# Kernel tuning notes

Measured on AMD Instinct MI355X. Metric: run time of the kernel, lower is better.

## Reference

```python
import jax, jax.numpy as jnp
import numpy as np

B, N_, K_, Q_, H = 32, 20, 10, 2048, 1024
EPS = 1e-5  # torch LayerNorm default


def setup_inputs() -> dict:
    key = jax.random.key(0)
    k1, k2 = jax.random.split(key)
    return {
        "support": jax.random.normal(k1, (B * N_ * K_, H), dtype=jnp.float32),
        "query": jax.random.normal(k2, (B * Q_, H), dtype=jnp.float32),
        "gamma": jnp.ones((H,), dtype=jnp.float32),
        "beta": jnp.zeros((H,), dtype=jnp.float32),
        "N": N_,
        "K": K_,
        "Q_total": Q_,
    }


def _layernorm(x, gamma, beta):
    m = jnp.mean(x, axis=-1, keepdims=True)
    v = jnp.mean(jnp.square(x - m), axis=-1, keepdims=True)  # biased variance
    return (x - m) * jax.lax.rsqrt(v + EPS) * gamma + beta


def reference(support, query, gamma, beta, N, K, Q_total):
    H_ = gamma.shape[0]
    s = _layernorm(support, gamma, beta).reshape(-1, N * K, H_)   # (B, NK, H)
    q = _layernorm(query, gamma, beta).reshape(-1, Q_total, H_)   # (B, Q, H)
    # broadcast dot-product similarity, fused as a batched matmul
    z = jnp.einsum("bqh,bkh->bqk", q, s)                          # (B, Q, NK)
    z = z.reshape(-1, Q_total, N, K)
    logits = jnp.max(z, axis=-1)                                  # max over K -> (B, Q, N)
    minn = jnp.min(logits, axis=-1)                               # min over N -> (B, Q)
    logits = jnp.concatenate([logits, minn[:, :, None] - 1.0], axis=2)  # (B, Q, N+1)
    pred = jnp.argmax(logits.reshape(-1, N + 1), axis=1)
    return logits, pred
```

## Files before the change

### kernel.cpp

```cpp
#include <hip/hip_runtime.h>
#include <hip/hip_bf16.h>

#define Hd   1024
#define Bd   32
#define Nd   20
#define Kd   10
#define NKd  200
#define NKP  208
#define Qd   2048
#define BM   128
#define ZR   64
#define ZLD  209
#define EPSf 1e-5f
#define TAU  0.02f
#define MAXF 2048
#define TCH  (832 * 8)
#define PLB  (TCH * 2)
#define BUFB (2 * PLB)

typedef __attribute__((ext_vector_type(8))) short bf16x8;
typedef __attribute__((ext_vector_type(4))) float f32x4;
typedef __attribute__((ext_vector_type(4))) unsigned int u32x4;

#define SWS(r) (((r) ^ ((r) >> 2)) & 3)

static __device__ __forceinline__ unsigned short f2bf(float f) {
  union { float f; unsigned u; } c; c.f = f;
  unsigned r = c.u + 0x7FFFu + ((c.u >> 16) & 1u);
  return (unsigned short)(r >> 16);
}
static __device__ __forceinline__ float bf2f(unsigned short h) {
  union { unsigned u; float f; } c; c.u = ((unsigned)h) << 16;
  return c.f;
}
static __device__ __forceinline__ float ubitf(unsigned u) {
  union { unsigned u; float f; } c; c.u = u; return c.f;
}
static __device__ __forceinline__ unsigned cvtpk_bf16(float a, float b) {
  unsigned r;
  asm("v_cvt_pk_bf16_f32 %0, %1, %2" : "=v"(r) : "v"(a), "v"(b));
  return r;
}
static __device__ __forceinline__ void gload_lds16(const void* g, void* l) {
  __builtin_amdgcn_global_load_lds(
      (const __attribute__((address_space(1))) unsigned int*)g,
      (__attribute__((address_space(3))) unsigned int*)l, 16, 0, 0);
}

__global__ __launch_bounds__(256) void ln_support(const float* __restrict__ x,
                                                  const float* __restrict__ gamma,
                                                  const float* __restrict__ beta,
                                                  unsigned short* __restrict__ y_hi,
                                                  unsigned short* __restrict__ y_lo,
                                                  float* __restrict__ Gv,
                                                  float* __restrict__ Bv) {
  int wave = threadIdx.x >> 6, lane = threadIdx.x & 63;
  int p = blockIdx.x * 4 + wave;
  int b = p / NKP, rr = p - b * NKP;
  int T0 = lane >> 1;
  int k8base = (lane & 1) * 2;
  int sw = SWS(rr);
  size_t chunkbase = (size_t)b * 32 * TCH + (size_t)T0 * TCH + (size_t)rr * 32;

  if (rr >= NKd) {
    bf16x8 z8 = {0, 0, 0, 0, 0, 0, 0, 0};
#pragma unroll
    for (int pr = 0; pr < 2; ++pr) {
      size_t off = chunkbase + (size_t)(((k8base + pr) ^ sw) * 8);
      *(bf16x8*)(y_hi + off) = z8;
      *(bf16x8*)(y_lo + off) = z8;
    }
    if (lane == 0) { Gv[p] = 0.f; Bv[p] = 0.f; }
    return;
  }
  const float4* xr = (const float4*)(x + ((size_t)b * NKd + rr) * Hd);
  const float4* gr = (const float4*)gamma;
  const float4* br = (const float4*)beta;
  float4 v[4];
  float s = 0.f, ss = 0.f;
#pragma unroll
  for (int j = 0; j < 4; ++j) {
    v[j] = xr[lane * 4 + j];
    s  += v[j].x + v[j].y + v[j].z + v[j].w;
    ss += v[j].x * v[j].x + v[j].y * v[j].y + v[j].z * v[j].z + v[j].w * v[j].w;
  }
#pragma unroll
  for (int o = 32; o; o >>= 1) { s += __shfl_xor(s, o, 64); ss += __shfl_xor(ss, o, 64); }
  float mean = s * (1.0f / Hd);
  float rstd = rsqrtf(ss * (1.0f / Hd) - mean * mean + EPSf);

  float nx[16];
  float sg = 0.f, sb = 0.f;
#pragma unroll
  for (int j = 0; j < 4; ++j) {
    float4 g = gr[lane * 4 + j], bb = br[lane * 4 + j];
    float xv[4] = {v[j].x, v[j].y, v[j].z, v[j].w};
    float gv4[4] = {g.x, g.y, g.z, g.w};
    float bv4[4] = {bb.x, bb.y, bb.z, bb.w};
#pragma unroll
    for (int e = 0; e < 4; ++e) {
      float n = (xv[e] - mean) * rstd * gv4[e] + bv4[e];
      nx[j * 4 + e] = n;
      sg += n * gv4[e];
      sb += n * bv4[e];
    }
  }
#pragma unroll
  for (int pr = 0; pr < 2; ++pr) {
    bf16x8 ph, pl;
#pragma unroll
    for (int e = 0; e < 8; ++e) {
      float n = nx[pr * 8 + e];
      unsigned short h = f2bf(n);
      ph[e] = (short)h;
      pl[e] = (short)f2bf(n - bf2f(h));
    }
    size_t off = chunkbase + (size_t)(((k8base + pr) ^ sw) * 8);
    *(bf16x8*)(y_hi + off) = ph;
    *(bf16x8*)(y_lo + off) = pl;
  }
#pragma unroll
  for (int o = 32; o; o >>= 1) { sg += __shfl_xor(sg, o, 64); sb += __shfl_xor(sb, o, 64); }
  if (lane == 0) { Gv[p] = sg; Bv[p] = sb; }
}

static __device__ __forceinline__ void split8(float4 xa, float4 xb, float4 ga, float4 gb,
                                              float& sx, float& sxx,
                                              bf16x8& AH, bf16x8& AL) {
  float x[8] = {xa.x, xa.y, xa.z, xa.w, xb.x, xb.y, xb.z, xb.w};
  float g[8] = {ga.x, ga.y, ga.z, ga.w, gb.x, gb.y, gb.z, gb.w};
  float u[8];
#pragma unroll
  for (int e = 0; e < 8; ++e) {
    sx += x[e];
    sxx = fmaf(x[e], x[e], sxx);
    u[e] = x[e] * g[e];
  }
  unsigned h[4], l[4];
#pragma unroll
  for (int p = 0; p < 4; ++p) {
    h[p] = cvtpk_bf16(u[2 * p], u[2 * p + 1]);
    float r0 = ubitf(h[p] << 16);
    float r1 = ubitf(h[p] & 0xFFFF0000u);
    l[p] = cvtpk_bf16(u[2 * p] - r0, u[2 * p + 1] - r1);
  }
  AH = __builtin_bit_cast(bf16x8, (u32x4){h[0], h[1], h[2], h[3]});
  AL = __builtin_bit_cast(bf16x8, (u32x4){l[0], l[1], l[2], l[3]});
}

__global__ __launch_bounds__(256, 2) void gemm_reduce(
    const float* __restrict__ query,
    const unsigned short* __restrict__ s_hi, const unsigned short* __restrict__ s_lo,
    const float* __restrict__ gamma,
    const float* __restrict__ Gv, const float* __restrict__ Bv,
    float* __restrict__ out_logits, float* __restrict__ out_pred,
    int* __restrict__ flag_cnt, int* __restrict__ flag_list) {
  __shared__ __align__(16) union {
    unsigned short B[2][2][TCH];
    float z[ZR][ZLD];
  } sm;

  int lin = blockIdx.x;
  int xcd = lin & 7, sl = lin >> 3;
  int b = xcd + 8 * (sl >> 4);
  int m0 = (sl & 15) * BM;
  int t = threadIdx.x;
  int wave = t >> 6, lane = t & 63;
  int m = lane & 15, quad = lane >> 4;

  const size_t qrow0 = (size_t)b * Qd + m0;
  const float* qf0 = query + (qrow0 + wave * 32 + m) * Hd;
  const float* qf1 = qf0 + 16 * Hd;
  const unsigned short* hb = s_hi + (size_t)b * 32 * TCH;
  const unsigned short* lb = s_lo + (size_t)b * 32 * TCH;

  char* ldsB = (char*)&sm.B[0][0][0];
  const char* rdB = ldsB + m * 64 + ((quad ^ SWS(m)) * 16);

  auto issue_dma = [&](int Tn, int bufsel) {
    size_t toff = (size_t)Tn * TCH;
    char* dstb = ldsB + bufsel * BUFB;
#pragma unroll
    for (int i = 0; i < 7; ++i) {
      int j = wave + i * 4;
      if (j < 26) {
        int pl = j >= 13 ? 1 : 0, jj = j - pl * 13;
        const unsigned short* src = (pl ? lb : hb) + toff + (size_t)jj * 512 + lane * 8;
        gload_lds16(src, dstb + pl * PLB + jj * 1024);
      }
    }
  };

  float4 xq00, xq01, xq10, xq11, gq0, gq1;
  auto loadA = [&](int T) {
    int ko = T * 32 + quad * 8;
    const float4* g4 = (const float4*)(gamma + ko);
    gq0 = g4[0]; gq1 = g4[1];
    const float4* q0 = (const float4*)(qf0 + ko);
    xq00 = q0[0]; xq01 = q0[1];
    const float4* q1 = (const float4*)(qf1 + ko);
    xq10 = q1[0]; xq11 = q1[1];
  };

  f32x4 acc0[13], acc1[13];
#pragma unroll
  for (int i = 0; i < 13; ++i) {
    acc0[i] = (f32x4){0.f, 0.f, 0.f, 0.f};
    acc1[i] = (f32x4){0.f, 0.f, 0.f, 0.f};
  }
  float sx0 = 0.f, sxx0 = 0.f, sx1 = 0.f, sxx1 = 0.f;

  issue_dma(0, 0);
  loadA(0);

  for (int T = 0; T < 32; ++T) {
    int u = T & 1;
    __syncthreads();

    if (T + 1 < 32) issue_dma(T + 1, 1 - u);

    bf16x8 ah0, al0, ah1, al1;
    split8(xq00, xq01, gq0, gq1, sx0, sxx0, ah0, al0);
    split8(xq10, xq11, gq0, gq1, sx1, sxx1, ah1, al1);
    if (T + 1 < 32) loadA(T + 1);

    const char* Bu = rdB + (u ? BUFB : 0);
#pragma unroll
    for (int nt = 0; nt < 13; ++nt) {
      bf16x8 bh = *(const bf16x8*)(Bu + nt * 1024);
      bf16x8 bl = *(const bf16x8*)(Bu + PLB + nt * 1024);
      acc0[nt] = __builtin_amdgcn_mfma_f32_16x16x32_bf16(ah0, bh, acc0[nt], 0, 0, 0);
      acc1[nt] = __builtin_amdgcn_mfma_f32_16x16x32_bf16(ah1, bh, acc1[nt], 0, 0, 0);
      acc0[nt] = __builtin_amdgcn_mfma_f32_16x16x32_bf16(al0, bh, acc0[nt], 0, 0, 0);
      acc1[nt] = __builtin_amdgcn_mfma_f32_16x16x32_bf16(al1, bh, acc1[nt], 0, 0, 0);
      acc0[nt] = __builtin_amdgcn_mfma_f32_16x16x32_bf16(ah0, bl, acc0[nt], 0, 0, 0);
      acc1[nt] = __builtin_amdgcn_mfma_f32_16x16x32_bf16(ah1, bl, acc1[nt], 0, 0, 0);
    }
  }

  sx0 += __shfl_xor(sx0, 16, 64);  sxx0 += __shfl_xor(sxx0, 16, 64);
  sx0 += __shfl_xor(sx0, 32, 64);  sxx0 += __shfl_xor(sxx0, 32, 64);
  sx1 += __shfl_xor(sx1, 16, 64);  sxx1 += __shfl_xor(sxx1, 16, 64);
  sx1 += __shfl_xor(sx1, 32, 64);  sxx1 += __shfl_xor(sxx1, 32, 64);
  float mean0 = sx0 * (1.0f / Hd);
  float rstd0 = rsqrtf(sxx0 * (1.0f / Hd) - mean0 * mean0 + EPSf);
  float mean1 = sx1 * (1.0f / Hd);
  float rstd1 = rsqrtf(sxx1 * (1.0f / Hd) - mean1 * mean1 + EPSf);

  float Gc[13], Bc[13];
#pragma unroll
  for (int nt = 0; nt < 13; ++nt) {
    int col = b * NKP + nt * 16 + m;
    Gc[nt] = Gv[col];
    Bc[nt] = Bv[col];
  }

#pragma unroll
  for (int pass = 0; pass < 2; ++pass) {
    __syncthreads();
    if ((wave >> 1) == pass) {
      int zb = (wave & 1) * 32;
#pragma unroll
      for (int r = 0; r < 4; ++r) {
        int lr = quad * 4 + r;
        {
          float mn = __shfl(mean0, lr, 16), rs = __shfl(rstd0, lr, 16);
          float mrs = mn * rs;
#pragma unroll
          for (int nt = 0; nt < 13; ++nt)
            sm.z[zb + lr][nt * 16 + m] = rs * acc0[nt][r] - mrs * Gc[nt] + Bc[nt];
        }
        {
          float mn = __shfl(mean1, lr, 16), rs = __shfl(rstd1, lr, 16);
          float mrs = mn * rs;
#pragma unroll
          for (int nt = 0; nt < 13; ++nt)
            sm.z[zb + 16 + lr][nt * 16 + m] = rs * acc1[nt][r] - mrs * Gc[nt] + Bc[nt];
        }
      }
    }
    __syncthreads();

    for (int i = t; i < ZR * Nd; i += 256) {
      int row = i / Nd, g = i - row * Nd;
      float* zp = &sm.z[row][g * Kd];
      float mx = zp[0];
#pragma unroll
      for (int j = 1; j < Kd; ++j) mx = fmaxf(mx, zp[j]);
      zp[0] = mx;
    }
    __syncthreads();

    if (t < ZR) {
      int row = t;
      float mn = 3.4e38f, v1 = -3.4e38f, v2 = -3.4e38f;
      int best = 0;
      size_t orow = qrow0 + pass * ZR + row;
      float* lp = out_logits + orow * (Nd + 1);
#pragma unroll
      for (int n = 0; n < Nd; ++n) {
        float v = sm.z[row][n * Kd];
        lp[n] = v;
        mn = fminf(mn, v);
        if (v > v1) { v2 = v1; v1 = v; best = n; }
        else v2 = fmaxf(v2, v);
      }
      lp[Nd] = mn - 1.0f;
      out_pred[orow] = (float)best;
      if (v1 - v2 < TAU) {
        int idx = atomicAdd(flag_cnt, 1);
        if (idx < MAXF) flag_list[idx] = (int)orow;
      }
    }
  }
}

__global__ __launch_bounds__(256) void refine_pred(
    const float* __restrict__ query, const float* __restrict__ support,
    const float* __restrict__ gamma, const float* __restrict__ beta,
    const int* __restrict__ flag_cnt, const int* __restrict__ flag_list,
    float* __restrict__ out_pred) {
  __shared__ double A[Hd];
  __shared__ double red[16];
  __shared__ double zbuf[NKd];
  __shared__ double gmax[Nd];
  int cnt = *flag_cnt; if (cnt > MAXF) cnt = MAXF;
  if ((int)blockIdx.x >= cnt) return;
  int qrow = flag_list[blockIdx.x];
  int b = qrow / Qd;
  int t = threadIdx.x, lane = t & 63, w = t >> 6;
  const float* qx = query + (size_t)qrow * Hd;
  float xv[4];
  double sx = 0.0, sxx = 0.0;
#pragma unroll
  for (int i = 0; i < 4; ++i) {
    xv[i] = qx[t * 4 + i];
    sx += (double)xv[i]; sxx += (double)xv[i] * (double)xv[i];
  }
#pragma unroll
  for (int o = 32; o; o >>= 1) { sx += __shfl_xor(sx, o, 64); sxx += __shfl_xor(sxx, o, 64); }
  if (lane == 0) { red[w] = sx; red[8 + w] = sxx; }
  __syncthreads();
  double m = (red[0] + red[1] + red[2] + red[3]) * (1.0 / Hd);
  double var = (red[8] + red[9] + red[10] + red[11]) * (1.0 / Hd) - m * m;
  double r = 1.0 / sqrt(var + 1e-5);
  double s1 = 0.0, s2 = 0.0;
#pragma unroll
  for (int i = 0; i < 4; ++i) {
    int j = t * 4 + i;
    double g = (double)gamma[j], be = (double)beta[j];
    double qn = ((double)xv[i] - m) * r * g + be;
    double a = qn * g;
    A[j] = a; s1 += a; s2 += qn * be;
  }
#pragma unroll
  for (int o = 32; o; o >>= 1) { s1 += __shfl_xor(s1, o, 64); s2 += __shfl_xor(s2, o, 64); }
  __syncthreads();
  if (lane == 0) { red[w] = s1; red[8 + w] = s2; }
  __syncthreads();
  double S1 = red[0] + red[1] + red[2] + red[3];
  double S2 = red[8] + red[9] + red[10] + red[11];
  const float* sbase = support + (size_t)b * NKd * Hd;
  for (int row = w; row < NKd; row += 4) {
    const float* xr = sbase + (size_t)row * Hd;
    double tx = 0.0, txx = 0.0, tax = 0.0;
#pragma unroll
    for (int i = 0; i < 16; ++i) {
      int j = lane + i * 64;
      double x = (double)xr[j];
      tx += x; txx += x * x; tax += A[j] * x;
    }
#pragma unroll
    for (int o = 32; o; o >>= 1) {
      tx += __shfl_xor(tx, o, 64); txx += __shfl_xor(txx, o, 64); tax += __shfl_xor(tax, o, 64);
    }
    if (lane == 0) {
      double mm = tx * (1.0 / Hd);
      double vv = txx * (1.0 / Hd) - mm * mm;
      double rr = 1.0 / sqrt(vv + 1e-5);
      zbuf[row] = rr * (tax - mm * S1) + S2;
    }
  }
  __syncthreads();
  if (t < Nd) {
    double mx = zbuf[t * Kd];
#pragma unroll
    for (int j = 1; j < Kd; ++j) mx = fmax(mx, zbuf[t * Kd + j]);
    gmax[t] = mx;
  }
  __syncthreads();
  if (t == 0) {
    double bv = gmax[0]; int best = 0;
#pragma unroll
    for (int n = 1; n < Nd; ++n) if (gmax[n] > bv) { bv = gmax[n]; best = n; }
    out_pred[qrow] = (float)best;
  }
}

extern "C" void kernel_launch(void* const* d_in, const int* in_sizes, int n_in,
                              void* d_out, int out_size, void* d_ws, size_t ws_size,
                              hipStream_t stream) {
  const float* support = (const float*)d_in[0];
  const float* query   = (const float*)d_in[1];
  const float* gamma   = (const float*)d_in[2];
  const float* beta    = (const float*)d_in[3];

  float* out = (float*)d_out;
  float* out_logits = out;
  float* out_pred   = out + (size_t)Bd * Qd * (Nd + 1);

  const size_t plane = (size_t)Bd * 32 * TCH;
  unsigned short* s_hi = (unsigned short*)d_ws;
  unsigned short* s_lo = s_hi + plane;
  char* p = (char*)(s_lo + plane);
  float* Gv = (float*)p;            p += (size_t)Bd * NKP * sizeof(float);
  float* Bv = (float*)p;            p += (size_t)Bd * NKP * sizeof(float);
  int* flag_cnt = (int*)p;
  int* flag_list = (int*)(p + 256);

  hipMemsetAsync(flag_cnt, 0, sizeof(int), stream);
  ln_support<<<(Bd * NKP) / 4, 256, 0, stream>>>(support, gamma, beta, s_hi, s_lo, Gv, Bv);
  gemm_reduce<<<Qd / BM * Bd, 256, 0, stream>>>(query, s_hi, s_lo, gamma, Gv, Bv,
                                                out_logits, out_pred, flag_cnt, flag_list);
  refine_pred<<<MAXF, 256, 0, stream>>>(query, support, gamma, beta, flag_cnt, flag_list, out_pred);
}
```

Baseline: 488.3 us.

## Triple-buffer support tiles with explicit vmcnt waits and prefetch distance two

```diff
diff --git a/kernel.cpp b/kernel.cpp
--- a/kernel.cpp
+++ b/kernel.cpp
@@ -156,9 +156,10 @@
     float* __restrict__ out_logits, float* __restrict__ out_pred,
     int* __restrict__ flag_cnt, int* __restrict__ flag_list) {
   __shared__ __align__(16) union {
-    unsigned short B[2][2][TCH];
+    unsigned short B[3][2][TCH];
     float z[ZR][ZLD];
   } sm;
+  __shared__ __align__(16) char dma_pad[1024];
 
   int lin = blockIdx.x;
   int xcd = lin & 7, sl = lin >> 3;
@@ -183,11 +184,12 @@
 #pragma unroll
     for (int i = 0; i < 7; ++i) {
       int j = wave + i * 4;
-      if (j < 26) {
-        int pl = j >= 13 ? 1 : 0, jj = j - pl * 13;
-        const unsigned short* src = (pl ? lb : hb) + toff + (size_t)jj * 512 + lane * 8;
-        gload_lds16(src, dstb + pl * PLB + jj * 1024);
-      }
+      bool real = (j < 26);
+      int pl = (real && j >= 13) ? 1 : 0;
+      int jj = real ? (j - pl * 13) : 0;
+      const unsigned short* src = (pl ? lb : hb) + toff + (size_t)jj * 512 + lane * 8;
+      void* dst = real ? (void*)(dstb + pl * PLB + jj * 1024) : (void*)dma_pad;
+      gload_lds16(src, dst);
     }
   };
 
@@ -211,20 +213,33 @@
   float sx0 = 0.f, sxx0 = 0.f, sx1 = 0.f, sxx1 = 0.f;
 
   issue_dma(0, 0);
+  __builtin_amdgcn_sched_barrier(0);
+  asm volatile("" ::: "memory");
   loadA(0);
-
+  __builtin_amdgcn_sched_barrier(0);
+  asm volatile("" ::: "memory");
+  issue_dma(1, 1);
+
+  int bu = 0;
   for (int T = 0; T < 32; ++T) {
-    int u = T & 1;
-    __syncthreads();
-
-    if (T + 1 < 32) issue_dma(T + 1, 1 - u);
+    if (T < 31) asm volatile("s_waitcnt vmcnt(13)" ::: "memory");
+    else        asm volatile("s_waitcnt vmcnt(6)" ::: "memory");
+    __builtin_amdgcn_s_barrier();
+    __builtin_amdgcn_sched_barrier(0);
 
     bf16x8 ah0, al0, ah1, al1;
     split8(xq00, xq01, gq0, gq1, sx0, sxx0, ah0, al0);
     split8(xq10, xq11, gq0, gq1, sx1, sxx1, ah1, al1);
     if (T + 1 < 32) loadA(T + 1);
-
-    const char* Bu = rdB + (u ? BUFB : 0);
+    __builtin_amdgcn_sched_barrier(0);
+    asm volatile("" ::: "memory");
+    if (T + 2 < 32) {
+      int bd = bu + 2; if (bd >= 3) bd -= 3;
+      issue_dma(T + 2, bd);
+    }
+
+    const char* Bu = rdB + bu * BUFB;
+    __builtin_amdgcn_s_setprio(1);
 #pragma unroll
     for (int nt = 0; nt < 13; ++nt) {
       bf16x8 bh = *(const bf16x8*)(Bu + nt * 1024);
@@ -236,6 +251,8 @@
       acc0[nt] = __builtin_amdgcn_mfma_f32_16x16x32_bf16(ah0, bl, acc0[nt], 0, 0, 0);
       acc1[nt] = __builtin_amdgcn_mfma_f32_16x16x32_bf16(ah1, bl, acc1[nt], 0, 0, 0);
     }
+    __builtin_amdgcn_s_setprio(0);
+    if (++bu == 3) bu = 0;
   }
 
   sx0 += __shfl_xor(sx0, 16, 64);  sxx0 += __shfl_xor(sxx0, 16, 64);
```

Result: slower. 499.8 us (+2.4%).

## Halve query tile per block, single-buffer LDS, raise occupancy to four blocks

Applied to the files above, without the earlier changes.

```diff
diff --git a/kernel.cpp b/kernel.cpp
--- a/kernel.cpp
+++ b/kernel.cpp
@@ -8,15 +8,14 @@
 #define NKd  200
 #define NKP  208
 #define Qd   2048
-#define BM   128
-#define ZR   64
+#define BM   64
+#define ZR   32
 #define ZLD  209
 #define EPSf 1e-5f
 #define TAU  0.02f
 #define MAXF 2048
 #define TCH  (832 * 8)
 #define PLB  (TCH * 2)
-#define BUFB (2 * PLB)
 
 typedef __attribute__((ext_vector_type(8))) short bf16x8;
 typedef __attribute__((ext_vector_type(4))) float f32x4;
@@ -148,7 +147,7 @@
   AL = __builtin_bit_cast(bf16x8, (u32x4){l[0], l[1], l[2], l[3]});
 }
 
-__global__ __launch_bounds__(256, 2) void gemm_reduce(
+__global__ __launch_bounds__(256, 4) void gemm_reduce(
     const float* __restrict__ query,
     const unsigned short* __restrict__ s_hi, const unsigned short* __restrict__ s_lo,
     const float* __restrict__ gamma,
@@ -156,96 +155,78 @@
     float* __restrict__ out_logits, float* __restrict__ out_pred,
     int* __restrict__ flag_cnt, int* __restrict__ flag_list) {
   __shared__ __align__(16) union {
-    unsigned short B[2][2][TCH];
+    unsigned short Bb[2][TCH];
     float z[ZR][ZLD];
   } sm;
 
   int lin = blockIdx.x;
   int xcd = lin & 7, sl = lin >> 3;
-  int b = xcd + 8 * (sl >> 4);
-  int m0 = (sl & 15) * BM;
+  int b = xcd + 8 * (sl >> 5);
+  int m0 = (sl & 31) * BM;
   int t = threadIdx.x;
   int wave = t >> 6, lane = t & 63;
   int m = lane & 15, quad = lane >> 4;
 
   const size_t qrow0 = (size_t)b * Qd + m0;
-  const float* qf0 = query + (qrow0 + wave * 32 + m) * Hd;
-  const float* qf1 = qf0 + 16 * Hd;
+  const float* qf0 = query + (qrow0 + wave * 16 + m) * Hd;
   const unsigned short* hb = s_hi + (size_t)b * 32 * TCH;
   const unsigned short* lb = s_lo + (size_t)b * 32 * TCH;
 
-  char* ldsB = (char*)&sm.B[0][0][0];
+  char* ldsB = (char*)&sm.Bb[0][0];
   const char* rdB = ldsB + m * 64 + ((quad ^ SWS(m)) * 16);
 
-  auto issue_dma = [&](int Tn, int bufsel) {
+  auto issue_dma = [&](int Tn) {
     size_t toff = (size_t)Tn * TCH;
-    char* dstb = ldsB + bufsel * BUFB;
-#pragma unroll
-    for (int i = 0; i < 7; ++i) {
-      int j = wave + i * 4;
-      if (j < 26) {
-        int pl = j >= 13 ? 1 : 0, jj = j - pl * 13;
-        const unsigned short* src = (pl ? lb : hb) + toff + (size_t)jj * 512 + lane * 8;
-        gload_lds16(src, dstb + pl * PLB + jj * 1024);
-      }
+    for (int j = wave; j < 26; j += 4) {
+      int pl = j >= 13 ? 1 : 0, jj = j - pl * 13;
+      const unsigned short* src = (pl ? lb : hb) + toff + (size_t)jj * 512 + lane * 8;
+      gload_lds16(src, ldsB + pl * PLB + jj * 1024);
     }
   };
 
-  float4 xq00, xq01, xq10, xq11, gq0, gq1;
+  float4 xq0, xq1, gq0, gq1;
   auto loadA = [&](int T) {
     int ko = T * 32 + quad * 8;
     const float4* g4 = (const float4*)(gamma + ko);
     gq0 = g4[0]; gq1 = g4[1];
     const float4* q0 = (const float4*)(qf0 + ko);
-    xq00 = q0[0]; xq01 = q0[1];
-    const float4* q1 = (const float4*)(qf1 + ko);
-    xq10 = q1[0]; xq11 = q1[1];
+    xq0 = q0[0]; xq1 = q0[1];
   };
 
-  f32x4 acc0[13], acc1[13];
-#pragma unroll
-  for (int i = 0; i < 13; ++i) {
-    acc0[i] = (f32x4){0.f, 0.f, 0.f, 0.f};
-    acc1[i] = (f32x4){0.f, 0.f, 0.f, 0.f};
-  }
-  float sx0 = 0.f, sxx0 = 0.f, sx1 = 0.f, sxx1 = 0.f;
-
-  issue_dma(0, 0);
+  f32x4 acc[13];
+#pragma unroll
+  for (int i = 0; i < 13; ++i) acc[i] = (f32x4){0.f, 0.f, 0.f, 0.f};
+  float sx = 0.f, sxx = 0.f;
+
+  issue_dma(0);
   loadA(0);
 
   for (int T = 0; T < 32; ++T) {
-    int u = T & 1;
-    __syncthreads();
-
-    if (T + 1 < 32) issue_dma(T + 1, 1 - u);
-
-    bf16x8 ah0, al0, ah1, al1;
-    split8(xq00, xq01, gq0, gq1, sx0, sxx0, ah0, al0);
-    split8(xq10, xq11, gq0, gq1, sx1, sxx1, ah1, al1);
+    __syncthreads();
+
+    bf16x8 ah, al;
+    split8(xq0, xq1, gq0, gq1, sx, sxx, ah, al);
     if (T + 1 < 32) loadA(T + 1);
 
-    const char* Bu = rdB + (u ? BUFB : 0);
+    __builtin_amdgcn_s_setprio(1);
 #pragma unroll
     for (int nt = 0; nt < 13; ++nt) {
-      bf16x8 bh = *(const bf16x8*)(Bu + nt * 1024);
-      bf16x8 bl = *(const bf16x8*)(Bu + PLB + nt * 1024);
-      acc0[nt] = __builtin_amdgcn_mfma_f32_16x16x32_bf16(ah0, bh, acc0[nt], 0, 0, 0);
-      acc1[nt] = __builtin_amdgcn_mfma_f32_16x16x32_bf16(ah1, bh, acc1[nt], 0, 0, 0);
-      acc0[nt] = __builtin_amdgcn_mfma_f32_16x16x32_bf16(al0, bh, acc0[nt], 0, 0, 0);
-      acc1[nt] = __builtin_amdgcn_mfma_f32_16x16x32_bf16(al1, bh, acc1[nt], 0, 0, 0);
-      acc0[nt] = __builtin_amdgcn_mfma_f32_16x16x32_bf16(ah0, bl, acc0[nt], 0, 0, 0);
-      acc1[nt] = __builtin_amdgcn_mfma_f32_16x16x32_bf16(ah1, bl, acc1[nt], 0, 0, 0);
-    }
-  }
-
-  sx0 += __shfl_xor(sx0, 16, 64);  sxx0 += __shfl_xor(sxx0, 16, 64);
-  sx0 += __shfl_xor(sx0, 32, 64);  sxx0 += __shfl_xor(sxx0, 32, 64);
-  sx1 += __shfl_xor(sx1, 16, 64);  sxx1 += __shfl_xor(sxx1, 16, 64);
-  sx1 += __shfl_xor(sx1, 32, 64);  sxx1 += __shfl_xor(sxx1, 32, 64);
-  float mean0 = sx0 * (1.0f / Hd);
-  float rstd0 = rsqrtf(sxx0 * (1.0f / Hd) - mean0 * mean0 + EPSf);
-  float mean1 = sx1 * (1.0f / Hd);
-  float rstd1 = rsqrtf(sxx1 * (1.0f / Hd) - mean1 * mean1 + EPSf);
+      bf16x8 bh = *(const bf16x8*)(rdB + nt * 1024);
+      bf16x8 bl = *(const bf16x8*)(rdB + PLB + nt * 1024);
+      acc[nt] = __builtin_amdgcn_mfma_f32_16x16x32_bf16(ah, bh, acc[nt], 0, 0, 0);
+      acc[nt] = __builtin_amdgcn_mfma_f32_16x16x32_bf16(al, bh, acc[nt], 0, 0, 0);
+      acc[nt] = __builtin_amdgcn_mfma_f32_16x16x32_bf16(ah, bl, acc[nt], 0, 0, 0);
+    }
+    __builtin_amdgcn_s_setprio(0);
+
+    __syncthreads();
+    if (T + 1 < 32) issue_dma(T + 1);
+  }
+
+  sx += __shfl_xor(sx, 16, 64);  sxx += __shfl_xor(sxx, 16, 64);
+  sx += __shfl_xor(sx, 32, 64);  sxx += __shfl_xor(sxx, 32, 64);
+  float mean = sx * (1.0f / Hd);
+  float rstd = rsqrtf(sxx * (1.0f / Hd) - mean * mean + EPSf);
 
   float Gc[13], Bc[13];
 #pragma unroll
@@ -259,24 +240,15 @@
   for (int pass = 0; pass < 2; ++pass) {
     __syncthreads();
     if ((wave >> 1) == pass) {
-      int zb = (wave & 1) * 32;
+      int zb = (wave & 1) * 16;
 #pragma unroll
       for (int r = 0; r < 4; ++r) {
         int lr = quad * 4 + r;
-        {
-          float mn = __shfl(mean0, lr, 16), rs = __shfl(rstd0, lr, 16);
-          float mrs = mn * rs;
-#pragma unroll
-          for (int nt = 0; nt < 13; ++nt)
-            sm.z[zb + lr][nt * 16 + m] = rs * acc0[nt][r] - mrs * Gc[nt] + Bc[nt];
-        }
-        {
-          float mn = __shfl(mean1, lr, 16), rs = __shfl(rstd1, lr, 16);
-          float mrs = mn * rs;
-#pragma unroll
-          for (int nt = 0; nt < 13; ++nt)
-            sm.z[zb + 16 + lr][nt * 16 + m] = rs * acc1[nt][r] - mrs * Gc[nt] + Bc[nt];
-        }
+        float mn = __shfl(mean, lr, 16), rs = __shfl(rstd, lr, 16);
+        float mrs = mn * rs;
+#pragma unroll
+        for (int nt = 0; nt < 13; ++nt)
+          sm.z[zb + lr][nt * 16 + m] = rs * acc[nt][r] - mrs * Gc[nt] + Bc[nt];
       }
     }
     __syncthreads();
```

Measured after the change: 490.8 us. About the same (+0.5%).

## Interleave DMA issue and MFMA phases with barriers and priority hints

Applied to the files above, without the earlier changes.

```diff
diff --git a/kernel.cpp b/kernel.cpp
--- a/kernel.cpp
+++ b/kernel.cpp
@@ -148,6 +148,8 @@
   AL = __builtin_bit_cast(bf16x8, (u32x4){l[0], l[1], l[2], l[3]});
 }
 
+#define MFMA_BF16 __builtin_amdgcn_mfma_f32_16x16x32_bf16
+
 __global__ __launch_bounds__(256, 2) void gemm_reduce(
     const float* __restrict__ query,
     const unsigned short* __restrict__ s_hi, const unsigned short* __restrict__ s_lo,
@@ -177,11 +179,11 @@
   char* ldsB = (char*)&sm.B[0][0][0];
   const char* rdB = ldsB + m * 64 + ((quad ^ SWS(m)) * 16);
 
-  auto issue_dma = [&](int Tn, int bufsel) {
+  auto issue_dma_phase = [&](int Tn, int bufsel, int p) {
     size_t toff = (size_t)Tn * TCH;
     char* dstb = ldsB + bufsel * BUFB;
 #pragma unroll
-    for (int i = 0; i < 7; ++i) {
+    for (int i = p; i < 7; i += 4) {
       int j = wave + i * 4;
       if (j < 26) {
         int pl = j >= 13 ? 1 : 0, jj = j - pl * 13;
@@ -210,31 +212,66 @@
   }
   float sx0 = 0.f, sxx0 = 0.f, sx1 = 0.f, sxx1 = 0.f;
 
-  issue_dma(0, 0);
+#pragma unroll
+  for (int p = 0; p < 4; ++p) issue_dma_phase(0, 0, p);
   loadA(0);
 
   for (int T = 0; T < 32; ++T) {
     int u = T & 1;
     __syncthreads();
 
-    if (T + 1 < 32) issue_dma(T + 1, 1 - u);
-
     bf16x8 ah0, al0, ah1, al1;
     split8(xq00, xq01, gq0, gq1, sx0, sxx0, ah0, al0);
     split8(xq10, xq11, gq0, gq1, sx1, sxx1, ah1, al1);
-    if (T + 1 < 32) loadA(T + 1);
 
     const char* Bu = rdB + (u ? BUFB : 0);
-#pragma unroll
-    for (int nt = 0; nt < 13; ++nt) {
-      bf16x8 bh = *(const bf16x8*)(Bu + nt * 1024);
-      bf16x8 bl = *(const bf16x8*)(Bu + PLB + nt * 1024);
-      acc0[nt] = __builtin_amdgcn_mfma_f32_16x16x32_bf16(ah0, bh, acc0[nt], 0, 0, 0);
-      acc1[nt] = __builtin_amdgcn_mfma_f32_16x16x32_bf16(ah1, bh, acc1[nt], 0, 0, 0);
-      acc0[nt] = __builtin_amdgcn_mfma_f32_16x16x32_bf16(al0, bh, acc0[nt], 0, 0, 0);
-      acc1[nt] = __builtin_amdgcn_mfma_f32_16x16x32_bf16(al1, bh, acc1[nt], 0, 0, 0);
-      acc0[nt] = __builtin_amdgcn_mfma_f32_16x16x32_bf16(ah0, bl, acc0[nt], 0, 0, 0);
-      acc1[nt] = __builtin_amdgcn_mfma_f32_16x16x32_bf16(ah1, bl, acc1[nt], 0, 0, 0);
+
+    {
+      bf16x8 bh[4], bl[4];
+#pragma unroll
+      for (int i = 0; i < 4; ++i) {
+        bh[i] = *(const bf16x8*)(Bu + i * 1024);
+        bl[i] = *(const bf16x8*)(Bu + PLB + i * 1024);
+      }
+      if (T + 1 < 32) { issue_dma_phase(T + 1, 1 - u, 0); loadA(T + 1); }
+      __builtin_amdgcn_s_barrier();
+      __builtin_amdgcn_sched_barrier(0);
+      __builtin_amdgcn_s_setprio(1);
+#pragma unroll
+      for (int i = 0; i < 4; ++i) {
+        acc0[i] = MFMA_BF16(ah0, bh[i], acc0[i], 0, 0, 0);
+        acc1[i] = MFMA_BF16(ah1, bh[i], acc1[i], 0, 0, 0);
+        acc0[i] = MFMA_BF16(al0, bh[i], acc0[i], 0, 0, 0);
+        acc1[i] = MFMA_BF16(al1, bh[i], acc1[i], 0, 0, 0);
+        acc0[i] = MFMA_BF16(ah0, bl[i], acc0[i], 0, 0, 0);
+        acc1[i] = MFMA_BF16(ah1, bl[i], acc1[i], 0, 0, 0);
+      }
+      __builtin_amdgcn_s_setprio(0);
+    }
+#pragma unroll
+    for (int p = 1; p < 4; ++p) {
+      int base = 1 + p * 3;
+      bf16x8 bh[3], bl[3];
+#pragma unroll
+      for (int i = 0; i < 3; ++i) {
+        bh[i] = *(const bf16x8*)(Bu + (base + i) * 1024);
+        bl[i] = *(const bf16x8*)(Bu + PLB + (base + i) * 1024);
+      }
+      if (T + 1 < 32) issue_dma_phase(T + 1, 1 - u, p);
+      __builtin_amdgcn_s_barrier();
+      __builtin_amdgcn_sched_barrier(0);
+      __builtin_amdgcn_s_setprio(1);
+#pragma unroll
+      for (int i = 0; i < 3; ++i) {
+        int nt = base + i;
+        acc0[nt] = MFMA_BF16(ah0, bh[i], acc0[nt], 0, 0, 0);
+        acc1[nt] = MFMA_BF16(ah1, bh[i], acc1[nt], 0, 0, 0);
+        acc0[nt] = MFMA_BF16(al0, bh[i], acc0[nt], 0, 0, 0);
+        acc1[nt] = MFMA_BF16(al1, bh[i], acc1[nt], 0, 0, 0);
+        acc0[nt] = MFMA_BF16(ah0, bl[i], acc0[nt], 0, 0, 0);
+        acc1[nt] = MFMA_BF16(ah1, bl[i], acc1[nt], 0, 0, 0);
+      }
+      __builtin_amdgcn_s_setprio(0);
     }
   }
 
```

After: 484.8 us. Within noise of the previous version (-0.7%).
